# Performance work log

Hardware: AMD Instinct MI355X
Metric: run time of the kernel (lower is better)

The kernel has to match this reference:

```python
import jax, jax.numpy as jnp
import numpy as np

N_ATOMS = 100000
N_EDGES = 6400000
R_MAX = 6.0
KE = 14.3996


def inverse_softplus(x):
    return np.log(np.expm1(x))


def setup_inputs() -> dict:
    key = jax.random.key(0)
    k_r, k_z, k_i, k_j = jax.random.split(key, 4)
    R = jax.random.normal(k_r, (N_ATOMS, 3), dtype=jnp.float32) * 10.0
    Z = jax.random.randint(k_z, (N_ATOMS,), 1, 50, dtype=jnp.int32)
    idx_i = jax.random.randint(k_i, (N_EDGES,), 0, N_ATOMS, dtype=jnp.int32)
    idx_j = jax.random.randint(k_j, (N_EDGES,), 0, N_ATOMS, dtype=jnp.int32)
    idx = jnp.stack([idx_i, idx_j], axis=0)  # [2, E]
    box = jnp.zeros((3,), dtype=jnp.float32)
    offsets = jnp.zeros((N_EDGES, 3), dtype=jnp.float32)
    # learned params stored in inverse-softplus space, as in setup()
    a_exp = jnp.full((1,), inverse_softplus(0.23), dtype=jnp.float32)
    a_num = jnp.full((1,), inverse_softplus(0.4685), dtype=jnp.float32)
    coefficients = jnp.asarray(
        inverse_softplus(np.array([0.18175, 0.50986, 0.28022, 0.02817])[:, None]),
        dtype=jnp.float32)
    exponents = jnp.asarray(
        inverse_softplus(np.array([3.1998, 0.94229, 0.4029, 0.20162])[:, None]),
        dtype=jnp.float32)
    rep_scale = jnp.full((1,), inverse_softplus(1.0 / KE), dtype=jnp.float32)
    return {"R": R, "Z": Z, "idx": idx, "box": box, "offsets": offsets,
            "a_exp": a_exp, "a_num": a_num, "coefficients": coefficients,
            "exponents": exponents, "rep_scale": rep_scale}


def reference(R, Z, idx, box, offsets, a_exp, a_num, coefficients, exponents, rep_scale):
    idx_i, idx_j = idx[0], idx[1]
    Zf = Z.astype(R.dtype)
    Z_i = Zf[idx_i]  # [E]
    Z_j = Zf[idx_j]  # [E]
    # free-space displacement: R[idx_j] - R[idx_i]  (box/offsets unused)
    dr_vec = R[idx_j] - R[idx_i]                     # [E, 3]
    dr = jnp.sqrt(jnp.sum(dr_vec * dr_vec, axis=-1))  # [E]
    dr = jnp.clip(dr, 0.02, R_MAX)
    cos_cutoff = 0.5 * (jnp.cos(np.pi * dr / R_MAX) + 1.0)
    sp = jax.nn.softplus
    ae = sp(a_exp)           # (1,)
    an = sp(a_num)           # (1,)
    c = sp(coefficients)     # (4, 1)
    e = sp(exponents)        # (4, 1)
    rs = sp(rep_scale)       # (1,)
    a_divisor = Z_i ** ae + Z_j ** ae              # [E]
    dist = dr * a_divisor / an                     # [E]
    f = jnp.sum(c * jnp.exp(-e * dist), axis=0)    # (4,E) -> [E]
    E_ij = Z_i * Z_j / dr * f * cos_cutoff         # [E]
    mask = (idx_i != idx_j).astype(E_ij.dtype)     # padded self-edges masked
    E = 0.5 * rs * KE * jnp.sum(E_ij * mask)       # (1,)
    return jnp.sum(E)                              # scalar
```

## Files before the change

kernel.cpp:

```cpp
#include <hip/hip_runtime.h>

#ifndef KE_CONST
#define KE_CONST 14.3996f
#endif

constexpr float R_MAX_C = 6.0f;
constexpr float LOG2E = 1.4426950408889634f;
constexpr float LN2 = 0.6931471805599453f;

__device__ __forceinline__ float fast_exp2(float x) { return __builtin_amdgcn_exp2f(x); }
__device__ __forceinline__ float fast_log2(float x) { return __builtin_amdgcn_logf(x); }
__device__ __forceinline__ float fast_exp(float x) { return __builtin_amdgcn_exp2f(x * LOG2E); }
__device__ __forceinline__ float cos_rev(float rev) { return __builtin_amdgcn_cosf(rev); }
__device__ __forceinline__ float fast_sqrt(float x) { return __builtin_amdgcn_sqrtf(x); }
__device__ __forceinline__ float fast_rcp(float x) { return __builtin_amdgcn_rcpf(x); }

__device__ __forceinline__ float softplus_f(float x) {
    return LN2 * fast_log2(1.0f + fast_exp(x));
}

__global__ void pack_atoms_kernel(const float* __restrict__ R,
                                  const int* __restrict__ Z,
                                  float4* __restrict__ atoms, int n) {
    int t = blockIdx.x * blockDim.x + threadIdx.x;
    if (t < n) {
        atoms[t] = make_float4(R[3 * t + 0], R[3 * t + 1], R[3 * t + 2],
                               (float)Z[t]);
    }
}

struct EdgeParams {
    float ae, inv_an, c0, c1, c2, c3, e0, e1, e2, e3;
};

__device__ __forceinline__ float edge_term(float xi, float yi, float zi, float zfi,
                                           float xj, float yj, float zj, float zfj,
                                           const EdgeParams& p) {
    float dx = xj - xi, dy = yj - yi, dz = zj - zi;
    float dr = fast_sqrt(dx * dx + dy * dy + dz * dz);
    dr = fminf(fmaxf(dr, 0.02f), R_MAX_C);
    float cc = 0.5f * (cos_rev(dr * (1.0f / 12.0f)) + 1.0f);
    float zpi = fast_exp2(p.ae * fast_log2(zfi));
    float zpj = fast_exp2(p.ae * fast_log2(zfj));
    float dist = dr * (zpi + zpj) * p.inv_an;
    float f = p.c0 * fast_exp(-p.e0 * dist) + p.c1 * fast_exp(-p.e1 * dist) +
              p.c2 * fast_exp(-p.e2 * dist) + p.c3 * fast_exp(-p.e3 * dist);
    return zfi * zfj * fast_rcp(dr) * f * cc;
}

template <bool PACKED>
__global__ __launch_bounds__(256) void edge_energy_kernel(
    const int* __restrict__ idx,
    const float4* __restrict__ atoms,
    const float* __restrict__ R,
    const int* __restrict__ Z,
    const float* __restrict__ a_exp, const float* __restrict__ a_num,
    const float* __restrict__ coefficients, const float* __restrict__ exponents,
    const float* __restrict__ rep_scale,
    float* __restrict__ out, int nEdges) {
    EdgeParams p;
    p.ae = softplus_f(a_exp[0]);
    p.inv_an = fast_rcp(softplus_f(a_num[0]));
    p.c0 = softplus_f(coefficients[0]);
    p.c1 = softplus_f(coefficients[1]);
    p.c2 = softplus_f(coefficients[2]);
    p.c3 = softplus_f(coefficients[3]);
    p.e0 = softplus_f(exponents[0]);
    p.e1 = softplus_f(exponents[1]);
    p.e2 = softplus_f(exponents[2]);
    p.e3 = softplus_f(exponents[3]);
    const float scale = 0.5f * softplus_f(rep_scale[0]) * KE_CONST;

    const int gid = blockIdx.x * blockDim.x + threadIdx.x;
    const int stride = gridDim.x * blockDim.x;
    const int nvec = nEdges >> 2;
    const int4* __restrict__ idx_i4 = (const int4*)idx;
    const int4* __restrict__ idx_j4 = (const int4*)(idx + nEdges);

    float acc = 0.0f;
    for (int k = gid; k < nvec; k += stride) {
        int4 ii = idx_i4[k];
        int4 jj = idx_j4[k];
        int iv[4] = {ii.x, ii.y, ii.z, ii.w};
        int jv[4] = {jj.x, jj.y, jj.z, jj.w};
#pragma unroll
        for (int u = 0; u < 4; ++u) {
            int i = iv[u], j = jv[u];
            float xi, yi, zi, zfi, xj, yj, zj, zfj;
            if (PACKED) {
                float4 ai = atoms[i];
                float4 aj = atoms[j];
                xi = ai.x; yi = ai.y; zi = ai.z; zfi = ai.w;
                xj = aj.x; yj = aj.y; zj = aj.z; zfj = aj.w;
            } else {
                xi = R[3 * i]; yi = R[3 * i + 1]; zi = R[3 * i + 2];
                xj = R[3 * j]; yj = R[3 * j + 1]; zj = R[3 * j + 2];
                zfi = (float)Z[i]; zfj = (float)Z[j];
            }
            float e = edge_term(xi, yi, zi, zfi, xj, yj, zj, zfj, p);
            acc += (i != j) ? e : 0.0f;
        }
    }
    for (int t = (nvec << 2) + gid; t < nEdges; t += stride) {
        int i = idx[t], j = idx[nEdges + t];
        float xi, yi, zi, zfi, xj, yj, zj, zfj;
        if (PACKED) {
            float4 ai = atoms[i];
            float4 aj = atoms[j];
            xi = ai.x; yi = ai.y; zi = ai.z; zfi = ai.w;
            xj = aj.x; yj = aj.y; zj = aj.z; zfj = aj.w;
        } else {
            xi = R[3 * i]; yi = R[3 * i + 1]; zi = R[3 * i + 2];
            xj = R[3 * j]; yj = R[3 * j + 1]; zj = R[3 * j + 2];
            zfi = (float)Z[i]; zfj = (float)Z[j];
        }
        float e = edge_term(xi, yi, zi, zfi, xj, yj, zj, zfj, p);
        acc += (i != j) ? e : 0.0f;
    }

#pragma unroll
    for (int off = 32; off > 0; off >>= 1) acc += __shfl_down(acc, off, 64);
    __shared__ float smem[4];
    const int lane = threadIdx.x & 63;
    const int wave = threadIdx.x >> 6;
    if (lane == 0) smem[wave] = acc;
    __syncthreads();
    if (threadIdx.x == 0) {
        float s = (smem[0] + smem[1]) + (smem[2] + smem[3]);
        atomicAdd(out, s * scale);
    }
}

extern "C" void kernel_launch(void* const* d_in, const int* in_sizes, int n_in,
                              void* d_out, int out_size, void* d_ws, size_t ws_size,
                              hipStream_t stream) {
    const float* R = (const float*)d_in[0];
    const int* Z = (const int*)d_in[1];
    const int* idx = (const int*)d_in[2];
    const float* a_exp = (const float*)d_in[5];
    const float* a_num = (const float*)d_in[6];
    const float* coefficients = (const float*)d_in[7];
    const float* exponents = (const float*)d_in[8];
    const float* rep_scale = (const float*)d_in[9];

    const int nAtoms = in_sizes[0] / 3;
    const int nEdges = in_sizes[2] / 2;
    float* out = (float*)d_out;

    (void)hipMemsetAsync(d_out, 0, sizeof(float), stream);

    const size_t need = (size_t)nAtoms * sizeof(float4);
    const int edge_blocks = 2048;
    if (ws_size >= need) {
        float4* atoms = (float4*)d_ws;
        pack_atoms_kernel<<<(nAtoms + 255) / 256, 256, 0, stream>>>(R, Z, atoms,
                                                                    nAtoms);
        edge_energy_kernel<true><<<edge_blocks, 256, 0, stream>>>(
            idx, atoms, R, Z, a_exp, a_num, coefficients, exponents, rep_scale,
            out, nEdges);
    } else {
        edge_energy_kernel<false><<<edge_blocks, 256, 0, stream>>>(
            idx, nullptr, R, Z, a_exp, a_num, coefficients, exponents, rep_scale,
            out, nEdges);
    }
}
```

Measured before the change: 204.7 us.

## Batch 8 edges per thread with nontemporal index loads and fold memset into pack

Replaces the grid-stride loop with a one-shot mapping where each thread loads 8 consecutive edge indices via nontemporal 16-byte loads, issues all 16 atom gathers up front, then computes. The grid grows to cover all edges (about 3125 blocks), launch bounds request 4 blocks per CU, and the output zeroing moves into the pack kernel, removing the separate memset. The fallback path for a small workspace is dropped, and the tail is handled by a serial loop in one thread. More gathers are in flight per thread, at the cost of higher register pressure.

```diff
diff --git a/kernel.cpp b/kernel.cpp
--- a/kernel.cpp
+++ b/kernel.cpp
@@ -7,6 +7,8 @@
 constexpr float R_MAX_C = 6.0f;
 constexpr float LOG2E = 1.4426950408889634f;
 constexpr float LN2 = 0.6931471805599453f;
+
+typedef int vint4 __attribute__((ext_vector_type(4)));
 
 __device__ __forceinline__ float fast_exp2(float x) { return __builtin_amdgcn_exp2f(x); }
 __device__ __forceinline__ float fast_log2(float x) { return __builtin_amdgcn_logf(x); }
@@ -21,8 +23,10 @@
 
 __global__ void pack_atoms_kernel(const float* __restrict__ R,
                                   const int* __restrict__ Z,
-                                  float4* __restrict__ atoms, int n) {
+                                  float4* __restrict__ atoms, int n,
+                                  float* __restrict__ out) {
     int t = blockIdx.x * blockDim.x + threadIdx.x;
+    if (t == 0) out[0] = 0.0f;
     if (t < n) {
         atoms[t] = make_float4(R[3 * t + 0], R[3 * t + 1], R[3 * t + 2],
                                (float)Z[t]);
@@ -33,31 +37,23 @@
     float ae, inv_an, c0, c1, c2, c3, e0, e1, e2, e3;
 };
 
-__device__ __forceinline__ float edge_term(float xi, float yi, float zi, float zfi,
-                                           float xj, float yj, float zj, float zfj,
+__device__ __forceinline__ float edge_term(const float4& ai, const float4& aj,
                                            const EdgeParams& p) {
-    float dx = xj - xi, dy = yj - yi, dz = zj - zi;
+    float dx = aj.x - ai.x, dy = aj.y - ai.y, dz = aj.z - ai.z;
     float dr = fast_sqrt(dx * dx + dy * dy + dz * dz);
     dr = fminf(fmaxf(dr, 0.02f), R_MAX_C);
     float cc = 0.5f * (cos_rev(dr * (1.0f / 12.0f)) + 1.0f);
-    float zpi = fast_exp2(p.ae * fast_log2(zfi));
-    float zpj = fast_exp2(p.ae * fast_log2(zfj));
+    float zpi = fast_exp2(p.ae * fast_log2(ai.w));
+    float zpj = fast_exp2(p.ae * fast_log2(aj.w));
     float dist = dr * (zpi + zpj) * p.inv_an;
     float f = p.c0 * fast_exp(-p.e0 * dist) + p.c1 * fast_exp(-p.e1 * dist) +
               p.c2 * fast_exp(-p.e2 * dist) + p.c3 * fast_exp(-p.e3 * dist);
-    return zfi * zfj * fast_rcp(dr) * f * cc;
+    return ai.w * aj.w * fast_rcp(dr) * f * cc;
 }
 
-template <bool PACKED>
-__global__ __launch_bounds__(256) void edge_energy_kernel(
-    const int* __restrict__ idx,
-    const float4* __restrict__ atoms,
-    const float* __restrict__ R,
-    const int* __restrict__ Z,
-    const float* __restrict__ a_exp, const float* __restrict__ a_num,
-    const float* __restrict__ coefficients, const float* __restrict__ exponents,
-    const float* __restrict__ rep_scale,
-    float* __restrict__ out, int nEdges) {
+__device__ __forceinline__ EdgeParams load_params(
+    const float* a_exp, const float* a_num, const float* coefficients,
+    const float* exponents) {
     EdgeParams p;
     p.ae = softplus_f(a_exp[0]);
     p.inv_an = fast_rcp(softplus_f(a_num[0]));
@@ -69,53 +65,51 @@
     p.e1 = softplus_f(exponents[1]);
     p.e2 = softplus_f(exponents[2]);
     p.e3 = softplus_f(exponents[3]);
+    return p;
+}
+
+__global__ __launch_bounds__(256, 4) void edge_energy_kernel(
+    const int* __restrict__ idx,
+    const float4* __restrict__ atoms,
+    const float* __restrict__ a_exp, const float* __restrict__ a_num,
+    const float* __restrict__ coefficients, const float* __restrict__ exponents,
+    const float* __restrict__ rep_scale,
+    float* __restrict__ out, int nEdges) {
+    EdgeParams p = load_params(a_exp, a_num, coefficients, exponents);
     const float scale = 0.5f * softplus_f(rep_scale[0]) * KE_CONST;
 
-    const int gid = blockIdx.x * blockDim.x + threadIdx.x;
-    const int stride = gridDim.x * blockDim.x;
-    const int nvec = nEdges >> 2;
-    const int4* __restrict__ idx_i4 = (const int4*)idx;
-    const int4* __restrict__ idx_j4 = (const int4*)(idx + nEdges);
+    const long long tid = (long long)blockIdx.x * blockDim.x + threadIdx.x;
+    const long long base = tid * 8;
 
     float acc = 0.0f;
-    for (int k = gid; k < nvec; k += stride) {
-        int4 ii = idx_i4[k];
-        int4 jj = idx_j4[k];
-        int iv[4] = {ii.x, ii.y, ii.z, ii.w};
-        int jv[4] = {jj.x, jj.y, jj.z, jj.w};
+    if (base + 8 <= (long long)nEdges) {
+        const vint4* __restrict__ i4 = (const vint4*)(idx) + (base >> 2);
+        const vint4* __restrict__ j4 = (const vint4*)(idx + nEdges) + (base >> 2);
+        vint4 ia = __builtin_nontemporal_load(i4);
+        vint4 ib = __builtin_nontemporal_load(i4 + 1);
+        vint4 ja = __builtin_nontemporal_load(j4);
+        vint4 jb = __builtin_nontemporal_load(j4 + 1);
+        int ii[8] = {ia.x, ia.y, ia.z, ia.w, ib.x, ib.y, ib.z, ib.w};
+        int jj[8] = {ja.x, ja.y, ja.z, ja.w, jb.x, jb.y, jb.z, jb.w};
+        float4 A[8], B[8];
 #pragma unroll
-        for (int u = 0; u < 4; ++u) {
-            int i = iv[u], j = jv[u];
-            float xi, yi, zi, zfi, xj, yj, zj, zfj;
-            if (PACKED) {
-                float4 ai = atoms[i];
-                float4 aj = atoms[j];
-                xi = ai.x; yi = ai.y; zi = ai.z; zfi = ai.w;
-                xj = aj.x; yj = aj.y; zj = aj.z; zfj = aj.w;
-            } else {
-                xi = R[3 * i]; yi = R[3 * i + 1]; zi = R[3 * i + 2];
-                xj = R[3 * j]; yj = R[3 * j + 1]; zj = R[3 * j + 2];
-                zfi = (float)Z[i]; zfj = (float)Z[j];
-            }
-            float e = edge_term(xi, yi, zi, zfi, xj, yj, zj, zfj, p);
+        for (int u = 0; u < 8; ++u) {
+            A[u] = atoms[ii[u]];
+            B[u] = atoms[jj[u]];
+        }
+#pragma unroll
+        for (int u = 0; u < 8; ++u) {
+            float e = edge_term(A[u], B[u], p);
+            acc += (ii[u] != jj[u]) ? e : 0.0f;
+        }
+    } else if (base < (long long)nEdges) {
+        for (long long t = base; t < (long long)nEdges; ++t) {
+            int i = idx[t], j = idx[nEdges + t];
+            float4 ai = atoms[i];
+            float4 aj = atoms[j];
+            float e = edge_term(ai, aj, p);
             acc += (i != j) ? e : 0.0f;
         }
-    }
-    for (int t = (nvec << 2) + gid; t < nEdges; t += stride) {
-        int i = idx[t], j = idx[nEdges + t];
-        float xi, yi, zi, zfi, xj, yj, zj, zfj;
-        if (PACKED) {
-            float4 ai = atoms[i];
-            float4 aj = atoms[j];
-            xi = ai.x; yi = ai.y; zi = ai.z; zfi = ai.w;
-            xj = aj.x; yj = aj.y; zj = aj.z; zfj = aj.w;
-        } else {
-            xi = R[3 * i]; yi = R[3 * i + 1]; zi = R[3 * i + 2];
-            xj = R[3 * j]; yj = R[3 * j + 1]; zj = R[3 * j + 2];
-            zfi = (float)Z[i]; zfj = (float)Z[j];
-        }
-        float e = edge_term(xi, yi, zi, zfi, xj, yj, zj, zfj, p);
-        acc += (i != j) ? e : 0.0f;
     }
 
 #pragma unroll
@@ -147,20 +141,12 @@
     const int nEdges = in_sizes[2] / 2;
     float* out = (float*)d_out;
 
-    (void)hipMemsetAsync(d_out, 0, sizeof(float), stream);
-
-    const size_t need = (size_t)nAtoms * sizeof(float4);
-    const int edge_blocks = 2048;
-    if (ws_size >= need) {
-        float4* atoms = (float4*)d_ws;
-        pack_atoms_kernel<<<(nAtoms + 255) / 256, 256, 0, stream>>>(R, Z, atoms,
-                                                                    nAtoms);
-        edge_energy_kernel<true><<<edge_blocks, 256, 0, stream>>>(
-            idx, atoms, R, Z, a_exp, a_num, coefficients, exponents, rep_scale,
-            out, nEdges);
-    } else {
-        edge_energy_kernel<false><<<edge_blocks, 256, 0, stream>>>(
-            idx, nullptr, R, Z, a_exp, a_num, coefficients, exponents, rep_scale,
-            out, nEdges);
-    }
+    float4* atoms = (float4*)d_ws;
+    pack_atoms_kernel<<<(nAtoms + 255) / 256, 256, 0, stream>>>(R, Z, atoms,
+                                                                nAtoms, out);
+    const int edges_per_block = 256 * 8;
+    const int blocks = (nEdges + edges_per_block - 1) / edges_per_block;
+    edge_energy_kernel<<<blocks, 256, 0, stream>>>(
+        idx, atoms, a_exp, a_num, coefficients, exponents, rep_scale, out,
+        nEdges);
 }
```

After: 204.3 us. About the same (-0.2%).
